# Optimization experiments

Hardware: AMD Instinct MI355X
Metric: run time of the kernel (lower is better)

## Reference

```python
import jax, jax.numpy as jnp
import numpy as np

B, N, FEAT, HID = 1024, 128, 512, 256


def setup_inputs() -> dict:
    key = jax.random.key(0)
    k1, k2, k3, k4, k5, k6 = jax.random.split(key, 6)
    x = jax.random.normal(k1, (B, FEAT), dtype=jnp.float32)
    labels = jax.random.randint(k2, (B,), 0, N, dtype=jnp.int64)
    W_proj = jax.random.normal(k3, (FEAT, HID), dtype=jnp.float32) / np.sqrt(FEAT)
    b_proj = jax.random.normal(k4, (HID,), dtype=jnp.float32) * 0.01
    means = jax.random.normal(k5, (N, HID), dtype=jnp.float32)
    # inverse covariances must be SPD so sqrt(dist_sq) is real
    A = jax.random.normal(k6, (N, HID, HID), dtype=jnp.float32)
    inv_covs = jnp.einsum('nij,nkj->nik', A, A) / HID + 0.1 * jnp.eye(HID, dtype=jnp.float32)
    return {"x": x, "labels": labels, "W_proj": W_proj, "b_proj": b_proj,
            "means": means, "inv_covs": inv_covs}


def reference(x, labels, W_proj, b_proj, means, inv_covs):
    b = x.shape[0]
    n = means.shape[0]
    x_proj = x @ W_proj + b_proj                       # (b, hid)
    delta = x_proj[:, None, :] - means[None, :, :]     # (b, n, hid)
    # batched Mahalanobis quadratic form
    dist_sq = jnp.einsum('bni,nij,bnj->bn', delta, inv_covs, delta)
    distmat = jnp.sqrt(dist_sq + 1e-12)                # (b, n)
    center_mask = (labels[:, None] == jnp.arange(n)[None, :]).astype(distmat.dtype)
    loss = jnp.clip(distmat * center_mask, 1e-12, 1e12).sum() / b
    return loss, distmat
```

## Files before the change

kernel.cpp:

```cpp
#include <hip/hip_runtime.h>
#include <hip/hip_bf16.h>

#define B_    1024
#define N_    128
#define FEAT_ 512
#define HID_  256

typedef __bf16 bf16x8 __attribute__((ext_vector_type(8)));
typedef float  f32x4  __attribute__((ext_vector_type(4)));

__device__ __forceinline__ unsigned int f2bf(float f) {
    unsigned int u = __float_as_uint(f);
    u += 0x7fffu + ((u >> 16) & 1u);
    return u >> 16;
}
__device__ __forceinline__ unsigned int pack2(float a, float b) {
    return f2bf(a) | (f2bf(b) << 16);
}

__global__ __launch_bounds__(512, 4) void prep_kernel(
    const float* __restrict__ x, const float* __restrict__ W,
    const float* __restrict__ bias, const float* __restrict__ means,
    const float* __restrict__ invcov,
    float* __restrict__ xp, unsigned short* __restrict__ xbf,
    unsigned short* __restrict__ Mbf, float* __restrict__ v2,
    float* __restrict__ cpart, float* __restrict__ out)
{
    __shared__ float smem[16 * FEAT_];
    const int t = threadIdx.x;
    if (blockIdx.x < 128) {
        float (*xs)[FEAT_] = (float (*)[FEAT_])smem;
        const int pb    = blockIdx.x;
        const int b0    = (pb >> 1) * 16;
        const int hbase = (pb & 1) * 128;
        {
            const float4* xsrc = (const float4*)(x + (size_t)b0 * FEAT_);
            #pragma unroll
            for (int i = 0; i < 4; ++i)
                ((float4*)smem)[t + i * 512] = xsrc[t + i * 512];
        }
        if (pb == 0 && t == 0) out[0] = (float)(N_ - 1) * 1e-12f;
        __syncthreads();
        const int w = t >> 6;
        const int l = t & 63;
        const float* __restrict__ xr0 = &xs[w * 2][0];
        const float* __restrict__ xr1 = &xs[w * 2 + 1][0];
        const float2* Wp = (const float2*)(W + hbase);
        float2 a0 = ((const float2*)(bias + hbase))[l];
        float2 a1 = a0;
        float2 Ab[8], Bb[8];
        auto LD = [&](float2 (&buf)[8], int g) {
            #pragma unroll
            for (int u = 0; u < 8; ++u) buf[u] = Wp[(size_t)(g * 8 + u) * 128 + l];
        };
        auto FM = [&](const float2 (&buf)[8], int g) {
            #pragma unroll
            for (int u = 0; u < 8; ++u) {
                const float x0 = xr0[g * 8 + u];
                const float x1 = xr1[g * 8 + u];
                a0.x += x0 * buf[u].x;  a0.y += x0 * buf[u].y;
                a1.x += x1 * buf[u].x;  a1.y += x1 * buf[u].y;
            }
        };
        LD(Ab, 0);
        for (int g = 0; g < 62; g += 2) {
            LD(Bb, g + 1);
            FM(Ab, g);
            LD(Ab, g + 2);
            FM(Bb, g + 1);
        }
        LD(Bb, 63);
        FM(Ab, 62);
        FM(Bb, 63);
        const int r0g = b0 + w * 2;
        ((float2*)(xp + (size_t)r0g * HID_ + hbase))[l]       = a0;
        ((float2*)(xp + (size_t)(r0g + 1) * HID_ + hbase))[l] = a1;
        *(unsigned int*)(xbf + (size_t)r0g * HID_ + hbase + l * 2)       = pack2(a0.x, a0.y);
        *(unsigned int*)(xbf + (size_t)(r0g + 1) * HID_ + hbase + l * 2) = pack2(a1.x, a1.y);
    } else {
        float (*sv)[33] = (float (*)[33])smem;
        float* sw = smem + 32 * 33;
        const int cb  = blockIdx.x - 128;
        const int n   = cb >> 3;
        const int jg2 = cb & 7;
        const float* Mn = invcov + (size_t)n * (HID_ * HID_) + (size_t)jg2 * 32 * HID_;
        const float* mu = means + (size_t)n * HID_;
        unsigned short* Mb = Mbf + (size_t)n * (HID_ * HID_) + (size_t)jg2 * 32 * HID_;
        const int gc = t & 31;
        const int r0 = t >> 5;
        const float4 mk0 = *(const float4*)(mu + gc * 8);
        const float4 mk1 = *(const float4*)(mu + gc * 8 + 4);
        #pragma unroll
        for (int i = 0; i < 2; ++i) {
            const int row = r0 + i * 16;
            const float* src = Mn + (size_t)row * HID_ + gc * 8;
            const float4 a = *(const float4*)src;
            const float4 b = *(const float4*)(src + 4);
            const int g2 = gc ^ ((row & 7) << 2);
            *(uint4*)(Mb + (size_t)row * HID_ + g2 * 8) =
                make_uint4(pack2(a.x, a.y), pack2(a.z, a.w), pack2(b.x, b.y), pack2(b.z, b.w));
            sv[row][gc] = a.x * mk0.x + a.y * mk0.y + a.z * mk0.z + a.w * mk0.w
                        + b.x * mk1.x + b.y * mk1.y + b.z * mk1.z + b.w * mk1.w;
        }
        __syncthreads();
        if (t < 256) {
            const int row = t >> 3;
            const int i0  = (t & 7) * 4;
            float v = sv[row][i0] + sv[row][i0 + 1] + sv[row][i0 + 2] + sv[row][i0 + 3];
            v += __shfl_xor(v, 1);
            v += __shfl_xor(v, 2);
            v += __shfl_xor(v, 4);
            const int j = jg2 * 32 + row;
            if ((t & 7) == 0) v2[(size_t)n * HID_ + j] = 2.f * v;
            float cc = ((t & 7) == 0) ? v * mu[j] : 0.f;
            cc += __shfl_xor(cc, 8);
            cc += __shfl_xor(cc, 16);
            cc += __shfl_xor(cc, 32);
            if ((t & 63) == 0) sw[t >> 6] = cc;
        }
        __syncthreads();
        if (t == 0) cpart[cb] = sw[0] + sw[1] + sw[2] + sw[3];
    }
}

__global__ __launch_bounds__(512, 4) void dist_kernel(
    const float* __restrict__ xp, const unsigned short* __restrict__ xbf,
    const unsigned short* __restrict__ Mbf, const float* __restrict__ v2,
    float* __restrict__ p)
{
    extern __shared__ unsigned short Ms[];

    const int tid  = threadIdx.x;
    const int bh   = blockIdx.x;
    const int jh   = blockIdx.y;
    const int n    = blockIdx.z;
    const int wave = tid >> 6;
    const int lane = tid & 63;
    const int q    = lane >> 4;
    const int l    = lane & 15;

    const unsigned short* src = Mbf + (size_t)n * (HID_ * HID_) + (size_t)jh * 32768;
    #pragma unroll
    for (int i = 0; i < 8; ++i) {
        const int c = i * 8 + wave;
        __builtin_amdgcn_global_load_lds(
            (const __attribute__((address_space(1))) unsigned int*)(src + (size_t)c * 512 + lane * 8),
            (__attribute__((address_space(3))) unsigned int*)&Ms[c * 512],
            16, 0, 0);
    }

    bf16x8 afrag[2][8];
    #pragma unroll
    for (int rb = 0; rb < 2; ++rb) {
        const unsigned short* xr = xbf + (size_t)(bh * 256 + wave * 32 + rb * 16 + l) * HID_;
        #pragma unroll
        for (int kk = 0; kk < 8; ++kk)
            afrag[rb][kk] = *(const bf16x8*)(xr + kk * 32 + q * 8);
    }
    float v2l[8];
    #pragma unroll
    for (int ct = 0; ct < 8; ++ct)
        v2l[ct] = v2[(size_t)n * HID_ + jh * 128 + ct * 16 + l];

    __syncthreads();

    float part[8];
    #pragma unroll
    for (int i = 0; i < 8; ++i) part[i] = 0.f;

    const size_t xbase = (size_t)(bh * 256 + wave * 32 + q * 4) * HID_ + jh * 128 + l;

    #pragma unroll
    for (int ct = 0; ct < 8; ++ct) {
        float xl[8];
        #pragma unroll
        for (int rb = 0; rb < 2; ++rb)
            #pragma unroll
            for (int r = 0; r < 4; ++r)
                xl[rb * 4 + r] = xp[xbase + (size_t)(rb * 16 + r) * HID_ + ct * 16];

        f32x4 acc0 = {0.f,0.f,0.f,0.f}, acc1 = {0.f,0.f,0.f,0.f};
        #pragma unroll
        for (int kk = 0; kk < 8; ++kk) {
            const bf16x8 bfrag = *(const bf16x8*)&Ms[(ct * 16 + l) * HID_ +
                                                     (((kk * 4 + q) ^ ((l & 7) << 2)) << 3)];
            acc0 = __builtin_amdgcn_mfma_f32_16x16x32_bf16(afrag[0][kk], bfrag, acc0, 0, 0, 0);
            acc1 = __builtin_amdgcn_mfma_f32_16x16x32_bf16(afrag[1][kk], bfrag, acc1, 0, 0, 0);
        }
        const float vv = v2l[ct];
        #pragma unroll
        for (int r = 0; r < 4; ++r) {
            part[r]     += (acc0[r] - vv) * xl[r];
            part[4 + r] += (acc1[r] - vv) * xl[4 + r];
        }
    }

    #pragma unroll
    for (int i = 0; i < 8; ++i) {
        float v = part[i];
        v += __shfl_xor(v, 1);
        v += __shfl_xor(v, 2);
        v += __shfl_xor(v, 4);
        v += __shfl_xor(v, 8);
        part[i] = v;
    }
    if (l == 0) {
        float* pb = p + (size_t)jh * (B_ * N_);
        #pragma unroll
        for (int i = 0; i < 8; ++i) {
            const int row = bh * 256 + wave * 32 + (i >> 2) * 16 + q * 4 + (i & 3);
            pb[(size_t)row * N_ + n] = part[i];
        }
    }
}

__global__ __launch_bounds__(256) void finalize_kernel(
    const float* __restrict__ p, const float* __restrict__ cpart,
    const int* __restrict__ labels, float* __restrict__ out)
{
    __shared__ float sc[128];
    __shared__ float ls[4];
    const int t = threadIdx.x;
    if (t < 128) {
        float s = 0.f;
        #pragma unroll
        for (int g = 0; g < 8; ++g) s += cpart[t * 8 + g];
        sc[t] = s;
    }
    __syncthreads();
    const int i = blockIdx.x * 256 + t;
    const int n = i & (N_ - 1);
    const int b = i >> 7;
    const float d = sqrtf(p[i] + p[B_ * N_ + i] + sc[n] + 1e-12f);
    out[1 + i] = d;
    float sel = (labels[b] == n) ? d : 0.f;
    #pragma unroll
    for (int m = 1; m <= 32; m <<= 1) sel += __shfl_xor(sel, m);
    if ((t & 63) == 0) ls[t >> 6] = sel;
    __syncthreads();
    if (t == 0) atomicAdd(out, (ls[0] + ls[1] + ls[2] + ls[3]) * (1.f / (float)B_));
}

extern "C" void kernel_launch(void* const* d_in, const int* in_sizes, int n_in,
                              void* d_out, int out_size, void* d_ws, size_t ws_size,
                              hipStream_t stream) {
    const float* x      = (const float*)d_in[0];
    const int*   labels = (const int*)d_in[1];
    const float* W      = (const float*)d_in[2];
    const float* bias   = (const float*)d_in[3];
    const float* means  = (const float*)d_in[4];
    const float* invcov = (const float*)d_in[5];
    float* out = (float*)d_out;

    char* ws = (char*)d_ws;
    unsigned short* Mbf   = (unsigned short*)(ws);
    float*          xp    = (float*)         (ws + 16777216);
    unsigned short* xbf   = (unsigned short*)(ws + 17825792);
    float*          v2    = (float*)         (ws + 18350080);
    float*          cpart = (float*)         (ws + 18481152);
    float*          p     = (float*)         (ws + 18489344);

    constexpr int DIST_LDS = 128 * HID_ * 2;
    (void)hipFuncSetAttribute((const void*)dist_kernel,
                              hipFuncAttributeMaxDynamicSharedMemorySize, DIST_LDS);

    prep_kernel<<<dim3(1152), 512, 0, stream>>>(x, W, bias, means, invcov,
                                                xp, xbf, Mbf, v2, cpart, out);
    dist_kernel<<<dim3(4, 2, N_), 512, DIST_LDS, stream>>>(xp, xbf, Mbf, v2, p);
    finalize_kernel<<<dim3((B_ * N_) / 256), 256, 0, stream>>>(p, cpart, labels, out);
}
```

Baseline: 154.4 us.

## Split projection GEMM into more blocks with one row per wave

The projection part of the prep kernel now uses 256 blocks of 8 rows instead of 128 blocks of 16, so each wave computes one output row instead of two. It reads x from LDS as float4, doubles the W prefetch depth to 16 rows, and pins the load/FMA interleave with sched_barriers. Occupancy is set through waves_per_eu instead of the launch-bounds minimum-blocks argument. The aim is more parallelism and better latency hiding on the projection blocks, at the cost of reading W twice as often in total and using more registers per thread.

After: 158.0 us. 1.02x slower.

```diff
diff --git a/kernel.cpp b/kernel.cpp
--- a/kernel.cpp
+++ b/kernel.cpp
@@ -18,7 +18,9 @@
     return f2bf(a) | (f2bf(b) << 16);
 }
 
-__global__ __launch_bounds__(512, 4) void prep_kernel(
+__global__ __launch_bounds__(512)
+__attribute__((amdgpu_waves_per_eu(4, 4)))
+void prep_kernel(
     const float* __restrict__ x, const float* __restrict__ W,
     const float* __restrict__ bias, const float* __restrict__ means,
     const float* __restrict__ invcov,
@@ -26,61 +28,64 @@
     unsigned short* __restrict__ Mbf, float* __restrict__ v2,
     float* __restrict__ cpart, float* __restrict__ out)
 {
-    __shared__ float smem[16 * FEAT_];
+    __shared__ float smem[8 * FEAT_];
     const int t = threadIdx.x;
-    if (blockIdx.x < 128) {
+    if (blockIdx.x < 256) {
         float (*xs)[FEAT_] = (float (*)[FEAT_])smem;
         const int pb    = blockIdx.x;
-        const int b0    = (pb >> 1) * 16;
+        const int b0    = (pb >> 1) * 8;
         const int hbase = (pb & 1) * 128;
         {
             const float4* xsrc = (const float4*)(x + (size_t)b0 * FEAT_);
-            #pragma unroll
-            for (int i = 0; i < 4; ++i)
-                ((float4*)smem)[t + i * 512] = xsrc[t + i * 512];
+            ((float4*)smem)[t]       = xsrc[t];
+            ((float4*)smem)[t + 512] = xsrc[t + 512];
         }
         if (pb == 0 && t == 0) out[0] = (float)(N_ - 1) * 1e-12f;
         __syncthreads();
         const int w = t >> 6;
         const int l = t & 63;
-        const float* __restrict__ xr0 = &xs[w * 2][0];
-        const float* __restrict__ xr1 = &xs[w * 2 + 1][0];
+        const float4* __restrict__ xr4 = (const float4*)&xs[w][0];
         const float2* Wp = (const float2*)(W + hbase);
-        float2 a0 = ((const float2*)(bias + hbase))[l];
-        float2 a1 = a0;
-        float2 Ab[8], Bb[8];
-        auto LD = [&](float2 (&buf)[8], int g) {
+        float2 acc = ((const float2*)(bias + hbase))[l];
+        float2 Ab[16], Bb[16];
+        auto LD = [&](float2 (&buf)[16], int g) {
             #pragma unroll
-            for (int u = 0; u < 8; ++u) buf[u] = Wp[(size_t)(g * 8 + u) * 128 + l];
+            for (int u = 0; u < 16; ++u) buf[u] = Wp[(size_t)(g * 16 + u) * 128 + l];
         };
-        auto FM = [&](const float2 (&buf)[8], int g) {
+        auto FM = [&](const float2 (&buf)[16], int g) {
             #pragma unroll
-            for (int u = 0; u < 8; ++u) {
-                const float x0 = xr0[g * 8 + u];
-                const float x1 = xr1[g * 8 + u];
-                a0.x += x0 * buf[u].x;  a0.y += x0 * buf[u].y;
-                a1.x += x1 * buf[u].x;  a1.y += x1 * buf[u].y;
+            for (int i = 0; i < 4; ++i) {
+                const float4 xv = xr4[g * 4 + i];
+                acc.x += xv.x * buf[i*4+0].x;  acc.y += xv.x * buf[i*4+0].y;
+                acc.x += xv.y * buf[i*4+1].x;  acc.y += xv.y * buf[i*4+1].y;
+                acc.x += xv.z * buf[i*4+2].x;  acc.y += xv.z * buf[i*4+2].y;
+                acc.x += xv.w * buf[i*4+3].x;  acc.y += xv.w * buf[i*4+3].y;
             }
         };
         LD(Ab, 0);
-        for (int g = 0; g < 62; g += 2) {
+        __builtin_amdgcn_sched_barrier(0);
+        for (int g = 0; g < 30; g += 2) {
             LD(Bb, g + 1);
+            __builtin_amdgcn_sched_barrier(0);
             FM(Ab, g);
+            __builtin_amdgcn_sched_barrier(0);
             LD(Ab, g + 2);
+            __builtin_amdgcn_sched_barrier(0);
             FM(Bb, g + 1);
-        }
-        LD(Bb, 63);
-        FM(Ab, 62);
-        FM(Bb, 63);
-        const int r0g = b0 + w * 2;
-        ((float2*)(xp + (size_t)r0g * HID_ + hbase))[l]       = a0;
-        ((float2*)(xp + (size_t)(r0g + 1) * HID_ + hbase))[l] = a1;
-        *(unsigned int*)(xbf + (size_t)r0g * HID_ + hbase + l * 2)       = pack2(a0.x, a0.y);
-        *(unsigned int*)(xbf + (size_t)(r0g + 1) * HID_ + hbase + l * 2) = pack2(a1.x, a1.y);
+            __builtin_amdgcn_sched_barrier(0);
+        }
+        LD(Bb, 31);
+        __builtin_amdgcn_sched_barrier(0);
+        FM(Ab, 30);
+        __builtin_amdgcn_sched_barrier(0);
+        FM(Bb, 31);
+        const int gr = b0 + w;
+        ((float2*)(xp + (size_t)gr * HID_ + hbase))[l] = acc;
+        *(unsigned int*)(xbf + (size_t)gr * HID_ + hbase + l * 2) = pack2(acc.x, acc.y);
     } else {
         float (*sv)[33] = (float (*)[33])smem;
         float* sw = smem + 32 * 33;
-        const int cb  = blockIdx.x - 128;
+        const int cb  = blockIdx.x - 256;
         const int n   = cb >> 3;
         const int jg2 = cb & 7;
         const float* Mn = invcov + (size_t)n * (HID_ * HID_) + (size_t)jg2 * 32 * HID_;
@@ -264,7 +269,7 @@
     (void)hipFuncSetAttribute((const void*)dist_kernel,
                               hipFuncAttributeMaxDynamicSharedMemorySize, DIST_LDS);
 
-    prep_kernel<<<dim3(1152), 512, 0, stream>>>(x, W, bias, means, invcov,
+    prep_kernel<<<dim3(1280), 512, 0, stream>>>(x, W, bias, means, invcov,
                                                 xp, xbf, Mbf, v2, cpart, out);
     dist_kernel<<<dim3(4, 2, N_), 512, DIST_LDS, stream>>>(xp, xbf, Mbf, v2, p);
     finalize_kernel<<<dim3((B_ * N_) / 256), 256, 0, stream>>>(p, cpart, labels, out);
```
